# Kernel optimization log

Measured on AMD Instinct MI355X. Metric: run time of the kernel, lower is better.

The kernel has to match this reference:

```python
import jax, jax.numpy as jnp
import numpy as np
from jax import lax

B, T, F = 64, 1536, 512
POOL = 6
UNITS = 256
NUM_CLASSES = 250


def _hard_sigmoid(x):
    # Keras hard_sigmoid: clip(0.2*x + 0.5, 0, 1)
    return jnp.clip(0.2 * x + 0.5, 0.0, 1.0)


def setup_inputs() -> dict:
    key = jax.random.key(0)
    ks = jax.random.split(key, 6)
    x = jax.random.normal(ks[0], (B, T, F), dtype=jnp.float32)
    # ConvLSTM1D with kernel_size=1 over a length-1 spatial axis == dense gates.
    W = jax.random.normal(ks[1], (F, 4 * UNITS), dtype=jnp.float32) * 0.05   # input kernel
    R = jax.random.normal(ks[2], (UNITS, 4 * UNITS), dtype=jnp.float32) * 0.05  # recurrent kernel
    b = jnp.zeros((4 * UNITS,), dtype=jnp.float32)
    Wd = jax.random.normal(ks[3], (UNITS, NUM_CLASSES), dtype=jnp.float32) * 0.05
    bd = jnp.zeros((NUM_CLASSES,), dtype=jnp.float32)
    return {"x": x, "W": W, "R": R, "b": b, "Wd": Wd, "bd": bd}


def reference(x, W, R, b, Wd, bd):
    Bx, Tx, Fx = x.shape
    Tp = Tx // POOL
    # AveragePooling1D(pool_size=6) over time
    xp = x[:, : Tp * POOL].reshape(Bx, Tp, POOL, Fx).mean(axis=2)  # [B, Tp, F]
    # Precompute input-to-gate contribution for all steps (one big GEMM)
    zx = jnp.einsum('btf,fg->btg', xp, W) + b  # [B, Tp, 4U]
    z_seq = jnp.swapaxes(zx, 0, 1)  # [Tp, B, 4U]

    h0 = jnp.zeros((Bx, UNITS), dtype=x.dtype)
    c0 = jnp.zeros((Bx, UNITS), dtype=x.dtype)

    def step(carry, z_t):
        h, c = carry
        z = z_t + h @ R  # [B, 4U]
        i, f, g, o = jnp.split(z, 4, axis=-1)  # Keras gate order: i, f, c, o
        i = _hard_sigmoid(i)
        f = _hard_sigmoid(f)
        g = jnp.tanh(g)
        o = _hard_sigmoid(o)
        c = f * c + i * g
        h = o * jnp.tanh(c)
        return (h, c), None

    (h, _), _ = lax.scan(step, (h0, c0), z_seq)
    # squeeze(-2) + dropout(eval: identity) + flatten -> [B, UNITS]
    logits = h @ Wd + bd
    return jax.nn.softmax(logits, axis=-1)
```

## Files before the change

kernel.cpp:

```cpp
#include <hip/hip_runtime.h>
#include <hip/hip_bf16.h>

#define BB 64
#define TT 1536
#define FF 512
#define TP 256
#define UU 256
#define GG 1024
#define NC 250

typedef _Float16 h2_t __attribute__((ext_vector_type(2)));
typedef _Float16 f16x8 __attribute__((ext_vector_type(8)));
typedef float f32x4 __attribute__((ext_vector_type(4)));

#if defined(__has_builtin)
#  if __has_builtin(__builtin_amdgcn_fdot2)
#    define FDOT2(a, b, c) __builtin_amdgcn_fdot2((a), (b), (c), false)
#  endif
#endif
#ifndef FDOT2
__device__ __forceinline__ float fdot2_fb(h2_t a, h2_t b, float c) {
    return c + (float)a[0] * (float)b[0] + (float)a[1] * (float)b[1];
}
#  define FDOT2(a, b, c) fdot2_fb((a), (b), (c))
#endif

#define BC(u) __builtin_bit_cast(h2_t, (u))

__device__ __forceinline__ float hsig(float z) {
    return fminf(fmaxf(fmaf(z, 0.2f, 0.5f), 0.0f), 1.0f);
}

__device__ __forceinline__ float ftanh(float x) {
    float ax = fabsf(x);
    float e = __expf(-2.0f * ax);
    float t = (1.0f - e) / (1.0f + e);
    return copysignf(t, x);
}

__device__ __forceinline__ void dot4(float& z, const uint4& r, const uint4& h) {
    z = FDOT2(BC(r.x), BC(h.x), z);
    z = FDOT2(BC(r.y), BC(h.y), z);
    z = FDOT2(BC(r.z), BC(h.z), z);
    z = FDOT2(BC(r.w), BC(h.w), z);
}

#if defined(__has_builtin) && __has_builtin(__builtin_amdgcn_mov_dpp)
template <int CTRL>
__device__ __forceinline__ float qperm(float v) {
    return __builtin_bit_cast(float,
        __builtin_amdgcn_mov_dpp(__builtin_bit_cast(int, v), CTRL, 0xf, 0xf, true));
}
#else
template <int CTRL>
__device__ __forceinline__ float qperm(float v) {
    return __shfl_xor(v, CTRL == 0xB1 ? 1 : 2, 64);
}
#endif

__global__ __launch_bounds__(256) void pool_kernel(const float* __restrict__ x,
                                                   _Float16* __restrict__ xph) {
    int idx = blockIdx.x * 256 + threadIdx.x;
    int f = idx & (FF - 1);
    int m = idx >> 9;
    int b = m >> 8;
    int tp = m & (TP - 1);
    const float* src = x + ((size_t)b * TT + (size_t)tp * 6) * FF + f;
    float s = 0.0f;
#pragma unroll
    for (int j = 0; j < 6; ++j) s += src[j * FF];
    xph[idx] = (_Float16)(s * (1.0f / 6.0f));
}

__global__ __launch_bounds__(256) void conv_wt(const float* __restrict__ W,
                                               _Float16* __restrict__ Wt) {
    int d = blockIdx.x * 256 + threadIdx.x;
    int n = d >> 9;
    int k = d & 511;
    Wt[d] = (_Float16)W[(size_t)k * GG + n];
}

__global__ __launch_bounds__(256) void conv_rq(const float* __restrict__ R,
                                               unsigned* __restrict__ Rq) {
    int d = blockIdx.x * 256 + threadIdx.x;
    int i = d & 3;
    int qt = d >> 2;
    int t = qt & 511;
    int q = qt >> 9;
    int g = t >> 2, s = t & 3;
    int c = 8 * g + (q >> 3);
    int p4 = q & 7;
    int k = 64 * s + 8 * p4 + 2 * i;
    h2_t p;
    p[0] = (_Float16)R[(size_t)k * GG + c];
    p[1] = (_Float16)R[(size_t)(k + 1) * GG + c];
    Rq[d] = __builtin_bit_cast(unsigned, p);
}

__global__ __launch_bounds__(256, 2) void gemm_zx_mfma(const _Float16* __restrict__ Ah,
                                                       const _Float16* __restrict__ Bt,
                                                       const float* __restrict__ bias,
                                                       float* __restrict__ C) {
    __shared__ _Float16 As[128 * 40];
    __shared__ _Float16 Bs[128 * 40];
    const int tid = threadIdx.x;
    const int bn = blockIdx.x * 128;
    const int bm = blockIdx.y * 128;
    const int wave = tid >> 6, lane = tid & 63;
    const int wm = (wave & 1) * 64, wn = (wave >> 1) * 64;
    const int l15 = lane & 15, q8 = (lane >> 4) * 8;
    const int srow = tid >> 1, shalf = tid & 1;

    f32x4 acc[4][4] = {};
    const uint4* ag = (const uint4*)(Ah + (size_t)(bm + srow) * FF);
    const uint4* bg = (const uint4*)(Bt + (size_t)(bn + srow) * FF);
    uint4* as_st = (uint4*)As + 5 * srow + 2 * shalf;
    uint4* bs_st = (uint4*)Bs + 5 * srow + 2 * shalf;

    for (int k0 = 0; k0 < FF; k0 += 32) {
        int qi = (k0 >> 3) + shalf * 2;
        uint4 a0 = ag[qi], a1 = ag[qi + 1];
        uint4 b0 = bg[qi], b1 = bg[qi + 1];
        __syncthreads();
        as_st[0] = a0; as_st[1] = a1;
        bs_st[0] = b0; bs_st[1] = b1;
        __syncthreads();
        f16x8 af[4], bf[4];
#pragma unroll
        for (int mt = 0; mt < 4; ++mt)
            af[mt] = *(const f16x8*)&As[(wm + 16 * mt + l15) * 40 + q8];
#pragma unroll
        for (int nt = 0; nt < 4; ++nt)
            bf[nt] = *(const f16x8*)&Bs[(wn + 16 * nt + l15) * 40 + q8];
#pragma unroll
        for (int mt = 0; mt < 4; ++mt)
#pragma unroll
            for (int nt = 0; nt < 4; ++nt)
                acc[mt][nt] = __builtin_amdgcn_mfma_f32_16x16x32_f16(af[mt], bf[nt],
                                                                    acc[mt][nt], 0, 0, 0);
    }
    const int rq = (lane >> 4) * 4;
#pragma unroll
    for (int nt = 0; nt < 4; ++nt) {
        int col = bn + wn + 16 * nt + l15;
        float bv = bias[col];
#pragma unroll
        for (int mt = 0; mt < 4; ++mt) {
#pragma unroll
            for (int r = 0; r < 4; ++r) {
                int row = bm + wm + 16 * mt + rq + r;
                C[(size_t)row * GG + col] = ((const float*)&acc[mt][nt])[r] + bv;
            }
        }
    }
}

__global__ __launch_bounds__(512, 2) void lstm_scan(const float* __restrict__ zx,
                                                    const uint4* __restrict__ Rq4,
                                                    float* __restrict__ hfin) {
    __shared__ uint4 Rl[6][512];
    __shared__ float zfull[GG];
    __shared__ __align__(16) uint4 h2s[36];
    const int b = blockIdx.x;
    const int t = threadIdx.x;
    const int g = t >> 2, s = t & 3;

    uint4 rv[50];
#pragma unroll
    for (int q = 0; q < 50; ++q) rv[q] = Rq4[q * 512 + t];
#pragma unroll
    for (int j = 0; j < 6; ++j) Rl[j][t] = Rq4[(50 + j) * 512 + t];
    if (t < 144) ((unsigned*)h2s)[t] = 0u;
    float c = 0.0f;
    const float* zrow = zx + (size_t)b * TP * GG;
    const uint4* sRq = Rq4 + 56 * 512 + t;
    const uint4* h4 = h2s;
    __syncthreads();

    for (int step = 0; step < TP; ++step) {
        uint4 st[8];
#pragma unroll
        for (int j = 0; j < 8; ++j) st[j] = sRq[j * 512];
        float zxi = 0.f, zxf = 0.f, zxg = 0.f, zxo = 0.f;
        if (t < UU) {
            const float* zr = zrow + (size_t)step * GG;
            zxi = zr[t]; zxf = zr[UU + t]; zxg = zr[2 * UU + t]; zxo = zr[3 * UU + t];
        }

        float z[8] = {};
#pragma unroll
        for (int p4 = 0; p4 < 8; ++p4) {
            uint4 hh = h4[9 * s + p4];
#pragma unroll
            for (int cc = 0; cc < 8; ++cc) {
                int q = cc * 8 + p4;
                if (q < 50)      dot4(z[cc], rv[q], hh);
                else if (q < 56) dot4(z[cc], Rl[q - 50][t], hh);
                else             dot4(z[cc], st[q - 56], hh);
            }
        }
#pragma unroll
        for (int cc = 0; cc < 8; ++cc) {
            z[cc] += qperm<0xB1>(z[cc]);
            z[cc] += qperm<0x4E>(z[cc]);
        }
        float w0 = s == 0 ? z[0] : s == 1 ? z[2] : s == 2 ? z[4] : z[6];
        float w1 = s == 0 ? z[1] : s == 1 ? z[3] : s == 2 ? z[5] : z[7];
        *(float2*)&zfull[8 * g + 2 * s] = make_float2(w0, w1);
        __syncthreads();
        if (t < UU) {
            float zi = zfull[t] + zxi;
            float zf = zfull[UU + t] + zxf;
            float zg = zfull[2 * UU + t] + zxg;
            float zo = zfull[3 * UU + t] + zxo;
            float ig = hsig(zi);
            float fg = hsig(zf);
            float gv = ftanh(zg);
            float og = hsig(zo);
            c = fmaf(fg, c, ig * gv);
            float h = og * ftanh(c);
            int s2 = t >> 6, pos = t & 63;
            ((_Float16*)h2s)[s2 * 72 + pos] = (_Float16)h;
            if (step == TP - 1) hfin[(size_t)b * UU + t] = h;
        }
        __syncthreads();
    }
}

__global__ __launch_bounds__(256) void dense_softmax(const float* __restrict__ hfin,
                                                     const float* __restrict__ Wd,
                                                     const float* __restrict__ bd,
                                                     float* __restrict__ out) {
    __shared__ __align__(16) float hbuf[UU];
    __shared__ float red[256];
    const int b = blockIdx.x;
    const int tid = threadIdx.x;
    hbuf[tid] = hfin[(size_t)b * UU + tid];
    __syncthreads();
    float logit = -3.0e38f;
    if (tid < NC) {
        float acc = bd[tid];
        for (int u = 0; u < UU; u += 4) {
            float4 hv = *(const float4*)&hbuf[u];
            acc = fmaf(hv.x, Wd[(size_t)(u + 0) * NC + tid], acc);
            acc = fmaf(hv.y, Wd[(size_t)(u + 1) * NC + tid], acc);
            acc = fmaf(hv.z, Wd[(size_t)(u + 2) * NC + tid], acc);
            acc = fmaf(hv.w, Wd[(size_t)(u + 3) * NC + tid], acc);
        }
        logit = acc;
    }
    red[tid] = logit;
    __syncthreads();
    for (int s = 128; s > 0; s >>= 1) {
        if (tid < s) red[tid] = fmaxf(red[tid], red[tid + s]);
        __syncthreads();
    }
    float mx = red[0];
    __syncthreads();
    float e = (tid < NC) ? expf(logit - mx) : 0.0f;
    red[tid] = e;
    __syncthreads();
    for (int s = 128; s > 0; s >>= 1) {
        if (tid < s) red[tid] += red[tid + s];
        __syncthreads();
    }
    if (tid < NC) out[(size_t)b * NC + tid] = e / red[0];
}

extern "C" void kernel_launch(void* const* d_in, const int* in_sizes, int n_in,
                              void* d_out, int out_size, void* d_ws, size_t ws_size,
                              hipStream_t stream) {
    const float* x  = (const float*)d_in[0];
    const float* W  = (const float*)d_in[1];
    const float* R  = (const float*)d_in[2];
    const float* bv = (const float*)d_in[3];
    const float* Wd = (const float*)d_in[4];
    const float* bd = (const float*)d_in[5];
    float* out = (float*)d_out;

    char* ws = (char*)d_ws;
    _Float16* xph = (_Float16*)ws;
    float* zx = (float*)(ws + 16777216);
    _Float16* Wt = (_Float16*)(ws + 83886080);
    unsigned* Rq = (unsigned*)(ws + 84934656);
    float* hfin = (float*)(ws + 85458944);

    hipLaunchKernelGGL(pool_kernel, dim3(32768), dim3(256), 0, stream, x, xph);
    hipLaunchKernelGGL(conv_wt, dim3(2048), dim3(256), 0, stream, W, Wt);
    hipLaunchKernelGGL(conv_rq, dim3(512), dim3(256), 0, stream, R, Rq);
    hipLaunchKernelGGL(gemm_zx_mfma, dim3(8, 128), dim3(256), 0, stream,
                       xph, Wt, bv, zx);
    hipLaunchKernelGGL(lstm_scan, dim3(64), dim3(512), 0, stream, zx,
                       (const uint4*)Rq, hfin);
    hipLaunchKernelGGL(dense_softmax, dim3(64), dim3(256), 0, stream, hfin, Wd, bd, out);
}
```

Baseline: 763.8 us.

## Restructure LSTM scan to two threads per unit with interleaved gate layout

The recurrent scan is reorganized so each pair of threads owns one hidden unit and computes all four gate dot products. The reduction now uses a single DPP step and avoids the shared zfull exchange, leaving one barrier per step instead of two. The input GEMM writes its output columns in a gate-interleaved permutation so each unit reads its four zx values as one prefetched float4. The pooling and weight-conversion kernels are vectorized, with a tiled shared-memory transpose replacing the strided per-element conversion. A double-buffered h avoids a read/write hazard, but the register and LDS split of R changes and occupancy pressure may shift.

After: 685.5 us. 1.11x faster.

```diff
diff --git a/kernel.cpp b/kernel.cpp
--- a/kernel.cpp
+++ b/kernel.cpp
@@ -61,40 +61,47 @@
 __global__ __launch_bounds__(256) void pool_kernel(const float* __restrict__ x,
                                                    _Float16* __restrict__ xph) {
     int idx = blockIdx.x * 256 + threadIdx.x;
-    int f = idx & (FF - 1);
-    int m = idx >> 9;
+    int f4 = (idx & 127) << 2;
+    int m = idx >> 7;
+    int tp = m & (TP - 1);
     int b = m >> 8;
-    int tp = m & (TP - 1);
-    const float* src = x + ((size_t)b * TT + (size_t)tp * 6) * FF + f;
-    float s = 0.0f;
-#pragma unroll
-    for (int j = 0; j < 6; ++j) s += src[j * FF];
-    xph[idx] = (_Float16)(s * (1.0f / 6.0f));
-}
-
-__global__ __launch_bounds__(256) void conv_wt(const float* __restrict__ W,
-                                               _Float16* __restrict__ Wt) {
-    int d = blockIdx.x * 256 + threadIdx.x;
-    int n = d >> 9;
-    int k = d & 511;
-    Wt[d] = (_Float16)W[(size_t)k * GG + n];
-}
-
-__global__ __launch_bounds__(256) void conv_rq(const float* __restrict__ R,
-                                               unsigned* __restrict__ Rq) {
-    int d = blockIdx.x * 256 + threadIdx.x;
-    int i = d & 3;
-    int qt = d >> 2;
-    int t = qt & 511;
-    int q = qt >> 9;
-    int g = t >> 2, s = t & 3;
-    int c = 8 * g + (q >> 3);
-    int p4 = q & 7;
-    int k = 64 * s + 8 * p4 + 2 * i;
-    h2_t p;
-    p[0] = (_Float16)R[(size_t)k * GG + c];
-    p[1] = (_Float16)R[(size_t)(k + 1) * GG + c];
-    Rq[d] = __builtin_bit_cast(unsigned, p);
+    const float* src = x + ((size_t)b * TT + (size_t)tp * 6) * FF + f4;
+    float sx = 0.f, sy = 0.f, sz = 0.f, sw = 0.f;
+#pragma unroll
+    for (int j = 0; j < 6; ++j) {
+        float4 v = *(const float4*)&src[j * FF];
+        sx += v.x; sy += v.y; sz += v.z; sw += v.w;
+    }
+    const float r6 = 1.0f / 6.0f;
+    h2_t lo, hi;
+    lo[0] = (_Float16)(sx * r6); lo[1] = (_Float16)(sy * r6);
+    hi[0] = (_Float16)(sz * r6); hi[1] = (_Float16)(sw * r6);
+    float2 w = make_float2(__builtin_bit_cast(float, lo), __builtin_bit_cast(float, hi));
+    *(float2*)&xph[(size_t)m * FF + f4] = w;
+}
+
+template <int PERM>
+__global__ __launch_bounds__(256) void transpose_cvt(const float* __restrict__ in,
+                                                     _Float16* __restrict__ out,
+                                                     int K, int N) {
+    __shared__ _Float16 tile[32][42];
+    const int r = threadIdx.x >> 3;
+    const int c4 = (threadIdx.x & 7) << 2;
+    const int n0 = blockIdx.x << 5;
+    const int k0 = blockIdx.y << 5;
+    float4 v = *(const float4*)&in[(size_t)(k0 + r) * N + n0 + c4];
+    tile[r][c4 + 0] = (_Float16)v.x;
+    tile[r][c4 + 1] = (_Float16)v.y;
+    tile[r][c4 + 2] = (_Float16)v.z;
+    tile[r][c4 + 3] = (_Float16)v.w;
+    __syncthreads();
+    int n = n0 + r;
+    int orow = PERM ? (((n & 255) << 2) | (n >> 8)) : n;
+    h2_t lo, hi;
+    lo[0] = tile[c4 + 0][r]; lo[1] = tile[c4 + 1][r];
+    hi[0] = tile[c4 + 2][r]; hi[1] = tile[c4 + 3][r];
+    float2 w = make_float2(__builtin_bit_cast(float, lo), __builtin_bit_cast(float, hi));
+    *(float2*)&out[(size_t)orow * K + k0 + c4] = w;
 }
 
 __global__ __launch_bounds__(256, 2) void gemm_zx_mfma(const _Float16* __restrict__ Ah,
@@ -143,7 +150,8 @@
 #pragma unroll
     for (int nt = 0; nt < 4; ++nt) {
         int col = bn + wn + 16 * nt + l15;
-        float bv = bias[col];
+        int oc = ((col & 3) << 8) | (col >> 2);
+        float bv = bias[oc];
 #pragma unroll
         for (int mt = 0; mt < 4; ++mt) {
 #pragma unroll
@@ -156,73 +164,70 @@
 }
 
 __global__ __launch_bounds__(512, 2) void lstm_scan(const float* __restrict__ zx,
-                                                    const uint4* __restrict__ Rq4,
+                                                    const _Float16* __restrict__ Rt,
                                                     float* __restrict__ hfin) {
-    __shared__ uint4 Rl[6][512];
-    __shared__ float zfull[GG];
-    __shared__ __align__(16) uint4 h2s[36];
+    __shared__ uint4 Rl[14][512];
+    __shared__ __align__(16) _Float16 hbuf[2][UU];
     const int b = blockIdx.x;
     const int t = threadIdx.x;
-    const int g = t >> 2, s = t & 3;
-
-    uint4 rv[50];
-#pragma unroll
-    for (int q = 0; q < 50; ++q) rv[q] = Rq4[q * 512 + t];
-#pragma unroll
-    for (int j = 0; j < 6; ++j) Rl[j][t] = Rq4[(50 + j) * 512 + t];
-    if (t < 144) ((unsigned*)h2s)[t] = 0u;
+    const int u = t >> 1, s = t & 1;
+
+    const uint4* rt = (const uint4*)Rt + (size_t)u * 32 + (s << 4);
+
+    uint4 rv[46];
+#pragma unroll
+    for (int g = 0; g < 4; ++g) {
+        const int RC = (g < 2) ? 12 : 11;
+        const int RO = (g == 0) ? 0 : (g == 1) ? 12 : (g == 2) ? 24 : 35;
+        const int LO = (g == 0) ? 0 : (g == 1) ? 3 : (g == 2) ? 6 : 10;
+#pragma unroll
+        for (int kk = 0; kk < 15; ++kk) {
+            if (kk < RC) rv[RO + kk] = rt[g * 8192 + kk];
+            else         Rl[LO + kk - RC][t] = rt[g * 8192 + kk];
+        }
+    }
+    if (t < 256) ((unsigned*)hbuf)[t] = 0u;
     float c = 0.0f;
-    const float* zrow = zx + (size_t)b * TP * GG;
-    const uint4* sRq = Rq4 + 56 * 512 + t;
-    const uint4* h4 = h2s;
-    __syncthreads();
-
+    const float4* zxp = (const float4*)zx + (size_t)b * TP * UU + u;
+    float4 zn = zxp[0];
+    __syncthreads();
+
+#pragma unroll 1
     for (int step = 0; step < TP; ++step) {
-        uint4 st[8];
-#pragma unroll
-        for (int j = 0; j < 8; ++j) st[j] = sRq[j * 512];
-        float zxi = 0.f, zxf = 0.f, zxg = 0.f, zxo = 0.f;
-        if (t < UU) {
-            const float* zr = zrow + (size_t)step * GG;
-            zxi = zr[t]; zxf = zr[UU + t]; zxg = zr[2 * UU + t]; zxo = zr[3 * UU + t];
-        }
-
-        float z[8] = {};
-#pragma unroll
-        for (int p4 = 0; p4 < 8; ++p4) {
-            uint4 hh = h4[9 * s + p4];
-#pragma unroll
-            for (int cc = 0; cc < 8; ++cc) {
-                int q = cc * 8 + p4;
-                if (q < 50)      dot4(z[cc], rv[q], hh);
-                else if (q < 56) dot4(z[cc], Rl[q - 50][t], hh);
-                else             dot4(z[cc], st[q - 56], hh);
+        float4 zn2 = zxp[(size_t)((step + 1 < TP) ? step + 1 : step) * UU];
+        uint4 st[4];
+#pragma unroll
+        for (int g = 0; g < 4; ++g) st[g] = rt[g * 8192 + 15];
+
+        const uint4* hq = (const uint4*)hbuf[step & 1] + (s << 4);
+        float z[4] = {0.f, 0.f, 0.f, 0.f};
+#pragma unroll
+        for (int kk = 0; kk < 16; ++kk) {
+            uint4 hh = hq[kk];
+#pragma unroll
+            for (int g = 0; g < 4; ++g) {
+                const int RC = (g < 2) ? 12 : 11;
+                const int RO = (g == 0) ? 0 : (g == 1) ? 12 : (g == 2) ? 24 : 35;
+                const int LO = (g == 0) ? 0 : (g == 1) ? 3 : (g == 2) ? 6 : 10;
+                if (kk < RC)      dot4(z[g], rv[RO + kk], hh);
+                else if (kk < 15) dot4(z[g], Rl[LO + kk - RC][t], hh);
+                else              dot4(z[g], st[g], hh);
             }
         }
 #pragma unroll
-        for (int cc = 0; cc < 8; ++cc) {
-            z[cc] += qperm<0xB1>(z[cc]);
-            z[cc] += qperm<0x4E>(z[cc]);
-        }
-        float w0 = s == 0 ? z[0] : s == 1 ? z[2] : s == 2 ? z[4] : z[6];
-        float w1 = s == 0 ? z[1] : s == 1 ? z[3] : s == 2 ? z[5] : z[7];
-        *(float2*)&zfull[8 * g + 2 * s] = make_float2(w0, w1);
-        __syncthreads();
-        if (t < UU) {
-            float zi = zfull[t] + zxi;
-            float zf = zfull[UU + t] + zxf;
-            float zg = zfull[2 * UU + t] + zxg;
-            float zo = zfull[3 * UU + t] + zxo;
-            float ig = hsig(zi);
-            float fg = hsig(zf);
-            float gv = ftanh(zg);
-            float og = hsig(zo);
-            c = fmaf(fg, c, ig * gv);
-            float h = og * ftanh(c);
-            int s2 = t >> 6, pos = t & 63;
-            ((_Float16*)h2s)[s2 * 72 + pos] = (_Float16)h;
-            if (step == TP - 1) hfin[(size_t)b * UU + t] = h;
-        }
+        for (int g = 0; g < 4; ++g) z[g] += qperm<0xB1>(z[g]);
+
+        float ig = hsig(z[0] + zn.x);
+        float fg = hsig(z[1] + zn.y);
+        float gv = ftanh(z[2] + zn.z);
+        float og = hsig(z[3] + zn.w);
+        c = fmaf(fg, c, ig * gv);
+        float h = og * ftanh(c);
+        if (s == 0) {
+            hbuf[(step + 1) & 1][u] = (_Float16)h;
+            if (step == TP - 1) hfin[(size_t)b * UU + u] = h;
+        }
+        zn = zn2;
         __syncthreads();
     }
 }
@@ -251,8 +256,8 @@
     }
     red[tid] = logit;
     __syncthreads();
-    for (int s = 128; s > 0; s >>= 1) {
-        if (tid < s) red[tid] = fmaxf(red[tid], red[tid + s]);
+    for (int sdx = 128; sdx > 0; sdx >>= 1) {
+        if (tid < sdx) red[tid] = fmaxf(red[tid], red[tid + sdx]);
         __syncthreads();
     }
     float mx = red[0];
@@ -260,8 +265,8 @@
     float e = (tid < NC) ? expf(logit - mx) : 0.0f;
     red[tid] = e;
     __syncthreads();
-    for (int s = 128; s > 0; s >>= 1) {
-        if (tid < s) red[tid] += red[tid + s];
+    for (int sdx = 128; sdx > 0; sdx >>= 1) {
+        if (tid < sdx) red[tid] += red[tid + sdx];
         __syncthreads();
     }
     if (tid < NC) out[(size_t)b * NC + tid] = e / red[0];
@@ -281,16 +286,17 @@
     char* ws = (char*)d_ws;
     _Float16* xph = (_Float16*)ws;
     float* zx = (float*)(ws + 16777216);
-    _Float16* Wt = (_Float16*)(ws + 83886080);
-    unsigned* Rq = (unsigned*)(ws + 84934656);
+    _Float16* Wtp = (_Float16*)(ws + 83886080);
+    _Float16* Rt  = (_Float16*)(ws + 84934656);
     float* hfin = (float*)(ws + 85458944);
 
-    hipLaunchKernelGGL(pool_kernel, dim3(32768), dim3(256), 0, stream, x, xph);
-    hipLaunchKernelGGL(conv_wt, dim3(2048), dim3(256), 0, stream, W, Wt);
-    hipLaunchKernelGGL(conv_rq, dim3(512), dim3(256), 0, stream, R, Rq);
+    hipLaunchKernelGGL(pool_kernel, dim3(8192), dim3(256), 0, stream, x, xph);
+    hipLaunchKernelGGL(HIP_KERNEL_NAME(transpose_cvt<1>), dim3(32, 16), dim3(256), 0,
+                       stream, W, Wtp, FF, GG);
+    hipLaunchKernelGGL(HIP_KERNEL_NAME(transpose_cvt<0>), dim3(32, 8), dim3(256), 0,
+                       stream, R, Rt, UU, GG);
     hipLaunchKernelGGL(gemm_zx_mfma, dim3(8, 128), dim3(256), 0, stream,
-                       xph, Wt, bv, zx);
-    hipLaunchKernelGGL(lstm_scan, dim3(64), dim3(512), 0, stream, zx,
-                       (const uint4*)Rq, hfin);
+                       xph, Wtp, bv, zx);
+    hipLaunchKernelGGL(lstm_scan, dim3(64), dim3(512), 0, stream, zx, Rt, hfin);
     hipLaunchKernelGGL(dense_softmax, dim3(64), dim3(256), 0, stream, hfin, Wd, bd, out);
 }
```
